# Optimization experiments

Hardware: AMD Instinct MI355X
Metric: run time of the kernel (lower is better)

Reference implementation:

```python
import jax, jax.numpy as jnp
import numpy as np
import math

D_MODEL = 1024
D_STATE = 64
DT_MIN = 0.001
DT_MAX = 0.1
BATCH = 4
SEQLEN = 4096


def make_hippo_matrix(N):
    P = np.sqrt(1 + 2 * np.arange(N))
    A = P[:, np.newaxis] * P[np.newaxis, :]
    A = np.tril(A) - np.diag(np.arange(N))
    return jnp.asarray(-A, dtype=jnp.float32)


def setup_inputs() -> dict:
    key = jax.random.key(0)
    k_u, k_B, k_C, k_D, k_dt = jax.random.split(key, 5)
    u = jax.random.normal(k_u, (BATCH, SEQLEN, D_MODEL), dtype=jnp.float32)
    A = make_hippo_matrix(D_STATE)  # (N, N) HiPPO-LegS buffer
    B = jax.random.normal(k_B, (D_STATE, 1), dtype=jnp.float32)
    C = jax.random.normal(k_C, (1, D_STATE), dtype=jnp.float32)
    D = jax.random.normal(k_D, (1,), dtype=jnp.float32)
    log_dt = (jax.random.uniform(k_dt, (1,), dtype=jnp.float32)
              * (math.log(DT_MAX) - math.log(DT_MIN)) + math.log(DT_MIN))
    return {"u": u, "A": A, "B": B, "C": C, "D": D, "log_dt": log_dt}


def _forward(u, A, B, C, D, log_dt):
    n = A.shape[0]
    dt = jnp.exp(log_dt)[0]
    A_bar = jax.scipy.linalg.expm(dt * A)                     # (N, N)
    B_bar = jnp.linalg.solve(A, (A_bar - jnp.eye(n, dtype=A.dtype)) @ B)  # (N, 1)
    bvec = B_bar[:, 0]          # (N,)
    cvec = C[0]                 # (N,)
    d_scalar = D[0]
    # Faithful to source: only channel 0 of u drives the SSM.
    u0 = u[:, :, 0]             # (Bn, L)

    def step(x, u_t):
        # x: (Bn, N), u_t: (Bn,)
        x = x @ A_bar.T + u_t[:, None] * bvec
        y = x @ cvec + d_scalar * u_t   # (Bn,)
        return x, y

    x0 = jnp.zeros((u.shape[0], n), dtype=u.dtype)
    _, ys = jax.lax.scan(step, x0, jnp.swapaxes(u0, 0, 1))   # (L, Bn)
    # Scalar output broadcast across all H channels (matches torch expand)
    y = jnp.broadcast_to(jnp.swapaxes(ys, 0, 1)[:, :, None], u.shape)
    return y


def reference(u, A, B, C, D, log_dt):
    return _forward(u, A, B, C, D, log_dt)
```

## Files before the change

### kernel.cpp

```cpp
#include <hip/hip_runtime.h>


#define NT 1024
#define MP 68
#define MSZ (64 * MP)
#define MOFF 4096
#define U0OFF (4096 + 8 * MSZ)

typedef __attribute__((ext_vector_type(8))) short v8s;
typedef __attribute__((ext_vector_type(4))) float v4f;

__device__ __forceinline__ unsigned short bf16r(float x) {
  union { float f; unsigned u; } v; v.f = x;
  unsigned r = v.u + 0x7fffu + ((v.u >> 16) & 1u);
  return (unsigned short)(r >> 16);
}
__device__ __forceinline__ float bf2f(unsigned short h) {
  union { unsigned u; float f; } v; v.u = ((unsigned)h) << 16;
  return v.f;
}

__device__ void mm_mfma(const float* gA, int aT, const float* gB, float* gC,
                        int pc, int nct, int colbase, unsigned short* FRAG) {
  const int t = threadIdx.x;
  __syncthreads();
  {
    const int slot = t >> 1;
    const int jh = (t & 1) * 4;
    const int l = slot & 63;
    const int Tq = slot >> 6;
    const int mrow = (Tq >> 1) * 16 + (l & 15);
    const int kk = (Tq & 1) * 32 + (l >> 4) * 8 + jh;
    float x0, x1, x2, x3;
    if (!aT) {
      const float4 f = *(const float4*)(gA + mrow * MP + kk);
      x0 = f.x; x1 = f.y; x2 = f.z; x3 = f.w;
    } else {
      x0 = gA[(kk + 0) * MP + mrow]; x1 = gA[(kk + 1) * MP + mrow];
      x2 = gA[(kk + 2) * MP + mrow]; x3 = gA[(kk + 3) * MP + mrow];
    }
    unsigned short h0 = bf16r(x0), h1 = bf16r(x1), h2 = bf16r(x2), h3 = bf16r(x3);
    ushort4 H, L;
    H.x = h0; H.y = h1; H.z = h2; H.w = h3;
    L.x = bf16r(x0 - bf2f(h0)); L.y = bf16r(x1 - bf2f(h1));
    L.z = bf16r(x2 - bf2f(h2)); L.w = bf16r(x3 - bf2f(h3));
    *(ushort4*)(FRAG + slot * 8 + jh) = H;
    *(ushort4*)(FRAG + 4096 + slot * 8 + jh) = L;
    const float y0 = gB[(kk + 0) * MP + mrow], y1 = gB[(kk + 1) * MP + mrow];
    const float y2 = gB[(kk + 2) * MP + mrow], y3 = gB[(kk + 3) * MP + mrow];
    unsigned short g0 = bf16r(y0), g1 = bf16r(y1), g2 = bf16r(y2), g3 = bf16r(y3);
    H.x = g0; H.y = g1; H.z = g2; H.w = g3;
    L.x = bf16r(y0 - bf2f(g0)); L.y = bf16r(y1 - bf2f(g1));
    L.z = bf16r(y2 - bf2f(g2)); L.w = bf16r(y3 - bf2f(g3));
    *(ushort4*)(FRAG + 8192 + slot * 8 + jh) = H;
    *(ushort4*)(FRAG + 12288 + slot * 8 + jh) = L;
  }
  __syncthreads();
  {
    const int w = t >> 6, l = t & 63;
    const int R = w >> 2, Cc = w & 3;
    if (Cc < nct) {
      const v8s Ah0 = *(const v8s*)(FRAG + ((R * 2 + 0) * 64 + l) * 8);
      const v8s Ah1 = *(const v8s*)(FRAG + ((R * 2 + 1) * 64 + l) * 8);
      const v8s Al0 = *(const v8s*)(FRAG + 4096 + ((R * 2 + 0) * 64 + l) * 8);
      const v8s Al1 = *(const v8s*)(FRAG + 4096 + ((R * 2 + 1) * 64 + l) * 8);
      const v8s Bh0 = *(const v8s*)(FRAG + 8192 + ((Cc * 2 + 0) * 64 + l) * 8);
      const v8s Bh1 = *(const v8s*)(FRAG + 8192 + ((Cc * 2 + 1) * 64 + l) * 8);
      const v8s Bl0 = *(const v8s*)(FRAG + 12288 + ((Cc * 2 + 0) * 64 + l) * 8);
      const v8s Bl1 = *(const v8s*)(FRAG + 12288 + ((Cc * 2 + 1) * 64 + l) * 8);
      v4f acc = {0.f, 0.f, 0.f, 0.f};
      acc = __builtin_amdgcn_mfma_f32_16x16x32_bf16(Ah0, Bh0, acc, 0, 0, 0);
      acc = __builtin_amdgcn_mfma_f32_16x16x32_bf16(Ah1, Bh1, acc, 0, 0, 0);
      acc = __builtin_amdgcn_mfma_f32_16x16x32_bf16(Ah0, Bl0, acc, 0, 0, 0);
      acc = __builtin_amdgcn_mfma_f32_16x16x32_bf16(Ah1, Bl1, acc, 0, 0, 0);
      acc = __builtin_amdgcn_mfma_f32_16x16x32_bf16(Al0, Bh0, acc, 0, 0, 0);
      acc = __builtin_amdgcn_mfma_f32_16x16x32_bf16(Al1, Bh1, acc, 0, 0, 0);
      const int col = colbase + Cc * 16 + (l & 15);
      const int r0 = R * 16 + (l >> 4) * 4;
      gC[(r0 + 0) * pc + col] = acc[0];
      gC[(r0 + 1) * pc + col] = acc[1];
      gC[(r0 + 2) * pc + col] = acc[2];
      gC[(r0 + 3) * pc + col] = acc[3];
    }
  }
  __syncthreads();
}

__device__ __forceinline__ void mv64(const float* Mm, const float* vin,
                                     float* vout, float* vscr) {
  __syncthreads();
  const int t = threadIdx.x, i = t & 63, c = t >> 6;
  const float4 m = *(const float4*)(Mm + i * MP + c * 4);
  vscr[t] = fmaf(m.x, vin[c * 4 + 0], fmaf(m.y, vin[c * 4 + 1],
            fmaf(m.z, vin[c * 4 + 2], m.w * vin[c * 4 + 3])));
  __syncthreads();
  if (t < 64) {
    float s = 0.f;
#pragma unroll
    for (int cc = 0; cc < 16; ++cc) s += vscr[cc * 64 + t];
    vout[t] = s;
  }
  __syncthreads();
}

__device__ void buildC(float* dst, const float* X, const float* X2, const float* X3,
                       float c0, float c1, float c2, float c3, int add) {
  __syncthreads();
  for (int e = threadIdx.x; e < 64 * MP; e += NT) {
    const int r = e / MP, c = e - r * MP;
    if (c < 64) {
      float v = c1 * X[e] + c2 * X2[e] + c3 * X3[e];
      if (c == r) v += c0;
      dst[e] = add ? dst[e] + v : v;
    }
  }
  __syncthreads();
}

__device__ __forceinline__ void ldscache(float* Lc, const float* gM) {
  __syncthreads();
  const int t = threadIdx.x;
  const int r = t >> 4, c4 = (t & 15) * 4;
  *(float4*)(Lc + r * MP + c4) = *(const float4*)(gM + r * MP + c4);
  __syncthreads();
}

__global__ __launch_bounds__(NT) void s4_setup(const float* __restrict__ u,
    const float* __restrict__ A, const float* __restrict__ Bv,
    const float* __restrict__ Cv, const float* __restrict__ logdt,
    float* __restrict__ ws) {
  if (blockIdx.x > 0) {
    const int idx = (blockIdx.x - 1) * NT + threadIdx.x;
    ws[U0OFF + idx] = u[(size_t)idx * 1024];
    return;
  }
  __shared__ __align__(16) unsigned short FRAG[16384];
  __shared__ float vscr[NT];
  __shared__ float va[64], vb[64], vg[64];
  __shared__ int s_s;
  float* Xc = (float*)FRAG;

  const int t = threadIdx.x;
  float* kbuf = ws;
  float* M0 = ws + MOFF;          float* M1 = M0 + MSZ;
  float* M2 = M1 + MSZ;           float* M3 = M2 + MSZ;
  float* M4 = M3 + MSZ;           float* M5 = M4 + MSZ;
  float* M6 = M5 + MSZ;           float* M7 = M6 + MSZ;
  const float dt = expf(logdt[0]);

  const float invf[17] = {1.f, 1.f, 1.f / 2.f, 1.f / 6.f, 1.f / 24.f, 1.f / 120.f,
                          1.f / 720.f, 1.f / 5040.f, 1.f / 40320.f, 1.f / 362880.f,
                          1.f / 3628800.f, 1.f / 39916800.f, 1.f / 479001600.f,
                          1.f / 6.2270208e9f, 1.f / 8.71782912e10f,
                          1.f / 1.307674368e12f, 1.f / 2.0922789888e13f};

  {
    const int j = t & 63, ch = t >> 6;
    float p = 0.f;
#pragma unroll
    for (int ii = 0; ii < 4; ++ii) p += fabsf(A[(ch * 4 + ii) * 64 + j]);
    vscr[t] = p;
    __syncthreads();
    if (t < 64) {
      float cs = 0.f;
#pragma unroll
      for (int c = 0; c < 16; ++c) cs += vscr[c * 64 + t];
      cs *= dt;
#pragma unroll
      for (int off = 32; off > 0; off >>= 1) cs = fmaxf(cs, __shfl_xor(cs, off));
      if (t == 0) {
        int s = 0;
        while (cs > 2.0f && s < 30) { cs *= 0.5f; ++s; }
        s_s = s;
      }
    }
    __syncthreads();
  }
  const int sq = s_s;
  const float scl = ldexpf(dt, -sq);

  {
    const float4 a4 = *(const float4*)(A + t * 4);
    float4 x;
    x.x = a4.x * scl; x.y = a4.y * scl; x.z = a4.z * scl; x.w = a4.w * scl;
    const int r = t >> 4, c4 = (t & 15) * 4;
    *(float4*)(M0 + r * MP + c4) = x;
    *(float4*)(Xc + r * MP + c4) = x;
  }
  __syncthreads();

  if (t < 64) { va[t] = Bv[t]; vg[t] = Bv[t]; }
  {
    float* vc = va; float* vn = vb;
    for (int k = 1; k <= 15; ++k) {
      mv64(Xc, vc, vn, vscr);
      if (t < 64) vg[t] = fmaf(vn[t], invf[k + 1], vg[t]);
      float* tmp = vc; vc = vn; vn = tmp;
    }
    __syncthreads();
  }

  mm_mfma(M0, 0, M0, M1, MP, 4, 0, FRAG);
  mm_mfma(M1, 0, M0, M2, MP, 4, 0, FRAG);
  mm_mfma(M1, 0, M1, M3, MP, 4, 0, FRAG);
  buildC(M5, M0, M1, M2, invf[12], invf[13], invf[14], invf[15], 0);
  mm_mfma(M5, 0, M3, M4, MP, 4, 0, FRAG);
  buildC(M4, M0, M1, M2, invf[8], invf[9], invf[10], invf[11], 1);
  mm_mfma(M4, 0, M3, M5, MP, 4, 0, FRAG);
  buildC(M5, M0, M1, M2, invf[4], invf[5], invf[6], invf[7], 1);
  mm_mfma(M5, 0, M3, M4, MP, 4, 0, FRAG);
  buildC(M4, M0, M1, M2, invf[0], invf[1], invf[2], invf[3], 1);

  float* F = M4; float* Fo = M5;
  for (int it = 0; it < sq; ++it) {
    mv64(F, vg, va, vscr);
    if (t < 64) vg[t] = 0.5f * (va[t] + vg[t]);
    mm_mfma(F, 0, F, Fo, MP, 4, 0, FRAG);
    float* tmp = F; F = Fo; Fo = tmp;
  }

  ldscache(Xc, F);
  if (t < 64) { va[t] = dt * vg[t]; M6[t * MP + 0] = dt * vg[t]; }
  __syncthreads();
  {
    float* vc = va; float* vn = vb;
    for (int r = 1; r < 16; ++r) {
      mv64(Xc, vc, vn, vscr);
      if (t < 64) M6[t * MP + r] = vn[t];
      float* tmp = vc; vc = vn; vn = tmp;
    }
    __syncthreads();
  }

  mm_mfma(F, 0, F, M0, MP, 4, 0, FRAG);
  mm_mfma(M0, 0, M0, M1, MP, 4, 0, FRAG);
  mm_mfma(M1, 0, M1, M0, MP, 4, 0, FRAG);
  mm_mfma(M0, 0, M0, M1, MP, 4, 0, FRAG);
  mm_mfma(M1, 0, M6, M6, MP, 1, 16, FRAG);
  mm_mfma(M1, 0, M1, M0, MP, 4, 0, FRAG);
  mm_mfma(M0, 0, M6, M6, MP, 2, 32, FRAG);
  mm_mfma(M0, 0, M0, M1, MP, 4, 0, FRAG);

  __syncthreads();
  for (int e = t; e < 4096; e += NT) {
    const int r = e >> 6, c = e & 63;
    Xc[c * MP + r] = M1[r * MP + c];
  }
  __syncthreads();
  if (t < 64) { va[t] = Cv[t]; M7[t * MP + 0] = Cv[t]; }
  __syncthreads();
  {
    float* vc = va; float* vn = vb;
    for (int q = 1; q < 16; ++q) {
      mv64(Xc, vc, vn, vscr);
      if (t < 64) M7[t * MP + q] = vn[t];
      float* tmp = vc; vc = vn; vn = tmp;
    }
    __syncthreads();
  }

  mm_mfma(M1, 0, M1, M0, MP, 4, 0, FRAG);
  mm_mfma(M0, 0, M0, M2, MP, 4, 0, FRAG);
  mm_mfma(M2, 0, M2, M0, MP, 4, 0, FRAG);
  mm_mfma(M0, 0, M0, M2, MP, 4, 0, FRAG);
  mm_mfma(M2, 1, M7, M7, MP, 1, 16, FRAG);
  mm_mfma(M2, 0, M2, M0, MP, 4, 0, FRAG);
  mm_mfma(M0, 1, M7, M7, MP, 2, 32, FRAG);

  mm_mfma(M7, 1, M6, kbuf, 64, 4, 0, FRAG);
}

__global__ __launch_bounds__(256) void s4_conv(const float* __restrict__ ws,
                                               const float* __restrict__ Dp,
                                               float* __restrict__ out) {
  __shared__ __align__(16) float ku[4096];
  __shared__ __align__(16) float uu[4096];
  const int b = blockIdx.x >> 6, m = blockIdx.x & 63;
  for (int i = threadIdx.x; i < 1024; i += 256) {
    ((float4*)ku)[i] = ((const float4*)ws)[i];
    ((float4*)uu)[i] = ((const float4*)(ws + U0OFF + b * 4096))[i];
  }
  __syncthreads();
  const float dsc = Dp[0];
  const int wv = threadIdx.x >> 6, lane = threadIdx.x & 63;
  const int c = m * 4 + wv;
#pragma unroll 1
  for (int i = 0; i < 16; ++i) {
    const int tt = c + 256 * i;
    float acc = 0.f;
    for (int j = lane; j <= tt; j += 64) acc = fmaf(ku[j], uu[tt - j], acc);
#pragma unroll
    for (int off = 32; off > 0; off >>= 1) acc += __shfl_xor(acc, off);
    if (lane == 0) out[(size_t)(b * 4096 + tt) * 1024] = acc + dsc * uu[tt];
  }
}

__global__ __launch_bounds__(256) void s4_bcast(float* __restrict__ out) {
  __shared__ float sy[4];
  const int row0 = blockIdx.x * 4;
  if (threadIdx.x < 4) sy[threadIdx.x] = out[(size_t)(row0 + threadIdx.x) * 1024];
  __syncthreads();
  const int i = threadIdx.x >> 6, l = threadIdx.x & 63;
  const float y = sy[i];
  const float4 y4 = make_float4(y, y, y, y);
  float4* dst = (float4*)(out + (size_t)(row0 + i) * 1024);
  dst[l] = y4; dst[l + 64] = y4; dst[l + 128] = y4; dst[l + 192] = y4;
}

extern "C" void kernel_launch(void* const* d_in, const int* in_sizes, int n_in,
                              void* d_out, int out_size, void* d_ws, size_t ws_size,
                              hipStream_t stream) {
  const float* u  = (const float*)d_in[0];
  const float* A  = (const float*)d_in[1];
  const float* B  = (const float*)d_in[2];
  const float* C  = (const float*)d_in[3];
  const float* D  = (const float*)d_in[4];
  const float* ld = (const float*)d_in[5];
  float* ws = (float*)d_ws;

  s4_setup<<<17, NT, 0, stream>>>(u, A, B, C, ld, ws);
  s4_conv<<<256, 256, 0, stream>>>(ws, D, (float*)d_out);
  s4_bcast<<<4096, 256, 0, stream>>>((float*)d_out);
}
```

Measured before the change: 200.3 us.

## Fuse causal convolution and channel broadcast into one output kernel

Merges the convolution kernel and the broadcast kernel into a single kernel. Each of 4096 blocks computes four consecutive output timesteps directly from global memory, reduces them across the block, and writes the broadcast rows itself. This drops one launch and the write-then-reread of column zero. In exchange the kernel and input vectors are re-read from global/L2 by every block without shared-memory staging, and the workload per block is uneven across timesteps. It also inlines a cache helper and drops one redundant barrier in setup.

```diff
diff --git a/kernel.cpp b/kernel.cpp
--- a/kernel.cpp
+++ b/kernel.cpp
@@ -117,14 +117,6 @@
   __syncthreads();
 }
 
-__device__ __forceinline__ void ldscache(float* Lc, const float* gM) {
-  __syncthreads();
-  const int t = threadIdx.x;
-  const int r = t >> 4, c4 = (t & 15) * 4;
-  *(float4*)(Lc + r * MP + c4) = *(const float4*)(gM + r * MP + c4);
-  __syncthreads();
-}
-
 __global__ __launch_bounds__(NT) void s4_setup(const float* __restrict__ u,
     const float* __restrict__ A, const float* __restrict__ Bv,
     const float* __restrict__ Cv, const float* __restrict__ logdt,
@@ -219,7 +211,11 @@
     float* tmp = F; F = Fo; Fo = tmp;
   }
 
-  ldscache(Xc, F);
+  __syncthreads();
+  {
+    const int r = t >> 4, c4 = (t & 15) * 4;
+    *(float4*)(Xc + r * MP + c4) = *(const float4*)(F + r * MP + c4);
+  }
   if (t < 64) { va[t] = dt * vg[t]; M6[t * MP + 0] = dt * vg[t]; }
   __syncthreads();
   {
@@ -270,40 +266,46 @@
   mm_mfma(M7, 1, M6, kbuf, 64, 4, 0, FRAG);
 }
 
-__global__ __launch_bounds__(256) void s4_conv(const float* __restrict__ ws,
-                                               const float* __restrict__ Dp,
-                                               float* __restrict__ out) {
-  __shared__ __align__(16) float ku[4096];
-  __shared__ __align__(16) float uu[4096];
-  const int b = blockIdx.x >> 6, m = blockIdx.x & 63;
-  for (int i = threadIdx.x; i < 1024; i += 256) {
-    ((float4*)ku)[i] = ((const float4*)ws)[i];
-    ((float4*)uu)[i] = ((const float4*)(ws + U0OFF + b * 4096))[i];
-  }
-  __syncthreads();
-  const float dsc = Dp[0];
-  const int wv = threadIdx.x >> 6, lane = threadIdx.x & 63;
-  const int c = m * 4 + wv;
-#pragma unroll 1
-  for (int i = 0; i < 16; ++i) {
-    const int tt = c + 256 * i;
-    float acc = 0.f;
-    for (int j = lane; j <= tt; j += 64) acc = fmaf(ku[j], uu[tt - j], acc);
-#pragma unroll
-    for (int off = 32; off > 0; off >>= 1) acc += __shfl_xor(acc, off);
-    if (lane == 0) out[(size_t)(b * 4096 + tt) * 1024] = acc + dsc * uu[tt];
-  }
-}
-
-__global__ __launch_bounds__(256) void s4_bcast(float* __restrict__ out) {
+__global__ __launch_bounds__(256) void s4_out(const float* __restrict__ ws,
+                                              const float* __restrict__ Dp,
+                                              float* __restrict__ out) {
+  const int bid = blockIdx.x;
+  const int b = bid >> 10;
+  const int t0 = (bid & 1023) << 2;
+  const float* kb = ws;
+  const float* ub = ws + U0OFF + (b << 12);
+  const int tid = threadIdx.x;
+  const int t3 = t0 + 3;
+  float a0 = 0.f, a1 = 0.f, a2 = 0.f, a3 = 0.f;
+  for (int j = tid; j <= t3; j += 256) {
+    const float kj = kb[j];
+    if (j <= t0)     a0 = fmaf(kj, ub[t0 - j], a0);
+    if (j <= t0 + 1) a1 = fmaf(kj, ub[t0 + 1 - j], a1);
+    if (j <= t0 + 2) a2 = fmaf(kj, ub[t0 + 2 - j], a2);
+    a3 = fmaf(kj, ub[t3 - j], a3);
+  }
+#pragma unroll
+  for (int off = 32; off > 0; off >>= 1) {
+    a0 += __shfl_xor(a0, off);
+    a1 += __shfl_xor(a1, off);
+    a2 += __shfl_xor(a2, off);
+    a3 += __shfl_xor(a3, off);
+  }
+  __shared__ float red[4][4];
   __shared__ float sy[4];
-  const int row0 = blockIdx.x * 4;
-  if (threadIdx.x < 4) sy[threadIdx.x] = out[(size_t)(row0 + threadIdx.x) * 1024];
-  __syncthreads();
-  const int i = threadIdx.x >> 6, l = threadIdx.x & 63;
-  const float y = sy[i];
+  if ((tid & 63) == 0) {
+    const int w = tid >> 6;
+    red[0][w] = a0; red[1][w] = a1; red[2][w] = a2; red[3][w] = a3;
+  }
+  __syncthreads();
+  if (tid < 4)
+    sy[tid] = red[tid][0] + red[tid][1] + red[tid][2] + red[tid][3] +
+              Dp[0] * ub[t0 + tid];
+  __syncthreads();
+  const int row = tid >> 6, l = tid & 63;
+  const float y = sy[row];
   const float4 y4 = make_float4(y, y, y, y);
-  float4* dst = (float4*)(out + (size_t)(row0 + i) * 1024);
+  float4* dst = (float4*)(out + ((size_t)(b << 12) + t0 + row) * 1024);
   dst[l] = y4; dst[l + 64] = y4; dst[l + 128] = y4; dst[l + 192] = y4;
 }
 
@@ -319,6 +321,5 @@
   float* ws = (float*)d_ws;
 
   s4_setup<<<17, NT, 0, stream>>>(u, A, B, C, ld, ws);
-  s4_conv<<<256, 256, 0, stream>>>(ws, D, (float*)d_out);
-  s4_bcast<<<4096, 256, 0, stream>>>((float*)d_out);
-}
+  s4_out<<<4096, 256, 0, stream>>>(ws, D, (float*)d_out);
+}
```

After: 182.2 us. -9.0%, faster.
